# Optimization experiments

Hardware: AMD Instinct MI355X
Metric: run time of the kernel (lower is better)

The kernel has to match this reference:

```python
import jax, jax.numpy as jnp
import numpy as np

B, N, C, H = 8, 1024, 768, 12
D = C // H
SCALE = D ** -0.5


def setup_inputs() -> dict:
    key = jax.random.key(0)
    ks = jax.random.split(key, 6)
    std = 0.02
    return {
        "x": jax.random.normal(ks[0], (B, N, C), dtype=jnp.float32),
        "w_qkv": jax.random.normal(ks[1], (3 * C, C), dtype=jnp.float32) * std,
        "w_proj": jax.random.normal(ks[2], (C, C), dtype=jnp.float32) * std,
        "b_proj": jnp.zeros((C,), dtype=jnp.float32),
        "conv_l_w": jax.random.normal(ks[3], (H, H), dtype=jnp.float32) * std,
        "conv_w_w": jax.random.normal(ks[4], (H, H), dtype=jnp.float32) * std,
    }


def reference(x, w_qkv, w_proj, b_proj, conv_l_w, conv_w_w):
    Bx, Nx, Cx = x.shape
    # qkv projection: torch Linear uses x @ W^T
    qkv = (x @ w_qkv.T).reshape(Bx, Nx, 3, H, D)
    qkv = jnp.transpose(qkv, (2, 0, 3, 1, 4))  # [3, B, H, N, D]
    q, k, v = qkv[0], qkv[1], qkv[2]
    q = q * SCALE
    attn = jnp.einsum("bhnd,bhmd->bhnm", q, k)  # [B,H,N,N]
    # 1x1 conv across heads (conv_l)
    attn = jnp.einsum("oh,bhnm->bonm", conv_l_w, attn)
    attn = jax.nn.softmax(attn, axis=-1)
    # 1x1 conv across heads (conv_w)
    attn = jnp.einsum("oh,bhnm->bonm", conv_w_w, attn)
    out = jnp.einsum("bhnm,bhmd->bhnd", attn, v)
    out = jnp.transpose(out, (0, 2, 1, 3)).reshape(Bx, Nx, Cx)
    return out @ w_proj.T + b_proj
```

## Files before the change

kernel.cpp:

```cpp
#include <hip/hip_runtime.h>
#include <hip/hip_bf16.h>

typedef __attribute__((ext_vector_type(8))) short short8;
typedef __attribute__((ext_vector_type(4))) short short4v;
typedef __attribute__((ext_vector_type(4))) float float4v;

#define NB 8
#define NH 12
#define NN 1024
#define ND 64
#define NC 768

__device__ __forceinline__ short f2bf(float f) {
  __hip_bfloat16 h = __float2bfloat16(f);
  union { __hip_bfloat16 h; short s; } u; u.h = h; return u.s;
}
__device__ __forceinline__ unsigned pk2(float a, float b) {
  unsigned ua = (unsigned short)f2bf(a);
  unsigned ub = (unsigned short)f2bf(b);
  return ua | (ub << 16);
}

template<int MODE>
__global__ __launch_bounds__(256, 2)
void gemm_kernel(const void* __restrict__ Ap, const float* __restrict__ Bw,
                 const float* __restrict__ bias,
                 __hip_bfloat16* __restrict__ Qo, __hip_bfloat16* __restrict__ Ko,
                 __hip_bfloat16* __restrict__ VTo, float* __restrict__ Out)
{
  __shared__ short As[128 * 40];
  __shared__ short Bs[128 * 40];
  const int tid = threadIdx.x;
  const int w = tid >> 6, lane = tid & 63, lr = lane & 15, lg = lane >> 4;
  const int wr = w >> 1, wc = w & 1;
  const int n0 = blockIdx.x * 128, m0 = blockIdx.y * 128;

  float4v acc[4][4];
  #pragma unroll
  for (int i = 0; i < 4; i++)
    #pragma unroll
    for (int j = 0; j < 4; j++)
      acc[i][j] = (float4v){0.f, 0.f, 0.f, 0.f};

  for (int kt = 0; kt < 768; kt += 32) {
    if (MODE == 0) {
      const float* A = (const float*)Ap;
      #pragma unroll
      for (int i2 = 0; i2 < 4; i2++) {
        int c = tid + 256 * i2;
        int row = c >> 3, c4 = c & 7;
        float4v v = *(const float4v*)(A + (size_t)(m0 + row) * 768 + kt + c4 * 4);
        short4v s = { f2bf(v[0]), f2bf(v[1]), f2bf(v[2]), f2bf(v[3]) };
        *(short4v*)(&As[row * 40 + c4 * 4]) = s;
      }
    } else {
      const __hip_bfloat16* A = (const __hip_bfloat16*)Ap;
      #pragma unroll
      for (int i2 = 0; i2 < 2; i2++) {
        int c = tid + 256 * i2;
        int row = c >> 2, c8 = c & 3;
        *(short8*)(&As[row * 40 + c8 * 8]) =
            *(const short8*)(A + (size_t)(m0 + row) * 768 + kt + c8 * 8);
      }
    }
    #pragma unroll
    for (int i2 = 0; i2 < 4; i2++) {
      int c = tid + 256 * i2;
      int row = c >> 3, c4 = c & 7;
      float4v v = *(const float4v*)(Bw + (size_t)(n0 + row) * 768 + kt + c4 * 4);
      short4v s = { f2bf(v[0]), f2bf(v[1]), f2bf(v[2]), f2bf(v[3]) };
      *(short4v*)(&Bs[row * 40 + c4 * 4]) = s;
    }
    __syncthreads();

    short8 af[4], bfr[4];
    #pragma unroll
    for (int i = 0; i < 4; i++)
      af[i] = *(const short8*)(&As[(wr * 64 + i * 16 + lr) * 40 + lg * 8]);
    #pragma unroll
    for (int j = 0; j < 4; j++)
      bfr[j] = *(const short8*)(&Bs[(wc * 64 + j * 16 + lr) * 40 + lg * 8]);
    #pragma unroll
    for (int i = 0; i < 4; i++)
      #pragma unroll
      for (int j = 0; j < 4; j++)
        acc[i][j] = __builtin_amdgcn_mfma_f32_16x16x32_bf16(af[i], bfr[j], acc[i][j], 0, 0, 0);
    __syncthreads();
  }

  #pragma unroll
  for (int i = 0; i < 4; i++) {
    #pragma unroll
    for (int j = 0; j < 4; j++) {
      #pragma unroll
      for (int r = 0; r < 4; r++) {
        float val = acc[i][j][r];
        int mg_ = m0 + wr * 64 + i * 16 + lg * 4 + r;
        int ng_ = n0 + wc * 64 + j * 16 + lr;
        if (MODE == 0) {
          int s = ng_ / 768;
          int rem = ng_ - s * 768;
          int h = rem >> 6, d = rem & 63;
          int b = mg_ >> 10, n = mg_ & 1023;
          if (s == 0)
            Qo[(((size_t)b * NH + h) * NN + n) * ND + d] = __float2bfloat16(val * 0.125f);
          else if (s == 1)
            Ko[(((size_t)b * NH + h) * NN + n) * ND + d] = __float2bfloat16(val);
          else
            VTo[(((size_t)b * NH + h) * ND + d) * NN + n] = __float2bfloat16(val);
        } else {
          Out[(size_t)mg_ * NC + ng_] = val + bias[ng_];
        }
      }
    }
  }
}

__global__ __launch_bounds__(256, 2)
void attn_kernel(const __hip_bfloat16* __restrict__ Qg, const __hip_bfloat16* __restrict__ Kg,
                 const __hip_bfloat16* __restrict__ VTg,
                 const float* __restrict__ convl, const float* __restrict__ convw,
                 __hip_bfloat16* __restrict__ AOut)
{
  __shared__ short Sb[32 * 576];
  __shared__ short pm[16 * 648];
  __shared__ short lwA[512];
  __shared__ short wwT[512];

  const int tid = threadIdx.x;
  const int w = tid >> 6, lane = tid & 63, lr = lane & 15, lg = lane >> 4;
  const int b = blockIdx.x & 7;
  const int n0 = (blockIdx.x >> 3) * 16;
  const float4v zf = (float4v){0.f, 0.f, 0.f, 0.f};

  for (int i = tid; i < 512; i += 256) {
    int r = i >> 5, k = i & 31;
    bool v = (r < 12) && (k < 12);
    lwA[i] = v ? f2bf(convl[r * 12 + k]) : (short)0;
    wwT[i] = v ? f2bf(convw[r * 12 + k]) : (short)0;
  }
  for (int i = tid; i < 512; i += 256) {
    short* p = &Sb[i * 36 + 12];
    #pragma unroll
    for (int j = 0; j < 24; j++) p[j] = 0;
  }

  short8 qf[3][2];
  #pragma unroll
  for (int hh = 0; hh < 3; hh++)
    #pragma unroll
    for (int ks = 0; ks < 2; ks++)
      qf[hh][ks] = *(const short8*)(Qg +
          (((size_t)b * NH + w * 3 + hh) * NN + n0 + lr) * ND + ks * 32 + lg * 8);

  short8 kreg[3][2][2];
  auto loadK = [&](int t) {
    const int m0t = t * 32;
    #pragma unroll
    for (int hh = 0; hh < 3; hh++) {
      const size_t kbase = (((size_t)b * NH + w * 3 + hh) * NN + m0t) * ND;
      #pragma unroll
      for (int j = 0; j < 2; j++)
        #pragma unroll
        for (int ks = 0; ks < 2; ks++)
          kreg[hh][j][ks] = *(const short8*)(Kg + kbase +
              (size_t)(j * 16 + lr) * ND + ks * 32 + lg * 8);
    }
  };
  loadK(0);
  __syncthreads();
  const short8 lwf = *(const short8*)(&lwA[lr * 32 + lg * 8]);
  const short8 wwf = *(const short8*)(&wwT[lr * 32 + lg * 8]);

  float Lacc[4][4];
  #pragma unroll
  for (int r = 0; r < 4; r++)
    #pragma unroll
    for (int nn = 0; nn < 4; nn++) Lacc[r][nn] = 0.f;

  for (int t = 0; t < 32; t++) {
    #pragma unroll
    for (int hh = 0; hh < 3; hh++) {
      const int h = w * 3 + hh;
      #pragma unroll
      for (int j = 0; j < 2; j++) {
        float4v a = zf;
        #pragma unroll
        for (int ks = 0; ks < 2; ks++)
          a = __builtin_amdgcn_mfma_f32_16x16x32_bf16(qf[hh][ks], kreg[hh][j][ks], a, 0, 0, 0);
        #pragma unroll
        for (int r = 0; r < 4; r++)
          Sb[((lg * 4 + r) * 2 + j) * 576 + lr * 36 + h] = f2bf(a[r]);
      }
    }
    loadK(t < 31 ? t + 1 : 0);
    __syncthreads();
    #pragma unroll
    for (int cc = 0; cc < 8; cc++) {
      const int c = w * 8 + cc;
      short8 sb = *(const short8*)(&Sb[c * 576 + lr * 36 + lg * 8]);
      float4v d = __builtin_amdgcn_mfma_f32_16x16x32_bf16(lwf, sb, zf, 0, 0, 0);
      #pragma unroll
      for (int r = 0; r < 4; r++)
        Lacc[r][cc >> 1] += __expf(d[r]);
    }
    __syncthreads();
  }
  float logLreg[4][4];
  #pragma unroll
  for (int r = 0; r < 4; r++)
    #pragma unroll
    for (int nn = 0; nn < 4; nn++) {
      float v = Lacc[r][nn];
      v += __shfl_xor(v, 1);
      v += __shfl_xor(v, 2);
      v += __shfl_xor(v, 4);
      v += __shfl_xor(v, 8);
      logLreg[r][nn] = __logf(v);
    }

  float4v oacc[3][4];
  #pragma unroll
  for (int hh = 0; hh < 3; hh++)
    #pragma unroll
    for (int jd = 0; jd < 4; jd++) oacc[hh][jd] = zf;

  for (int t = 0; t <= 32; t++) {
    short8 vt0[3][2];
    if (t > 0) {
      const int m0v = (t - 1) * 32;
      #pragma unroll
      for (int hh = 0; hh < 3; hh++) {
        const size_t vbase = ((size_t)b * NH + w * 3 + hh) * ND * NN;
        #pragma unroll
        for (int jj = 0; jj < 2; jj++)
          vt0[hh][jj] = *(const short8*)(VTg + vbase +
              (size_t)(jj * 16 + lr) * NN + m0v + lg * 8);
      }
    }
    if (t < 32) {
      #pragma unroll
      for (int hh = 0; hh < 3; hh++) {
        const int h = w * 3 + hh;
        #pragma unroll
        for (int j = 0; j < 2; j++) {
          float4v a = zf;
          #pragma unroll
          for (int ks = 0; ks < 2; ks++)
            a = __builtin_amdgcn_mfma_f32_16x16x32_bf16(qf[hh][ks], kreg[hh][j][ks], a, 0, 0, 0);
          #pragma unroll
          for (int r = 0; r < 4; r++)
            Sb[((lg * 4 + r) * 2 + j) * 576 + lr * 36 + h] = f2bf(a[r]);
        }
      }
      if (t < 31) loadK(t + 1);
    }
    if (t > 0) {
      const int m0v = (t - 1) * 32;
      short8 pf[3];
      #pragma unroll
      for (int hh = 0; hh < 3; hh++)
        pf[hh] = *(const short8*)(&pm[(w * 3 + hh) * 648 + lr * 40 + lg * 8]);
      #pragma unroll
      for (int hh = 0; hh < 3; hh++)
        #pragma unroll
        for (int jj = 0; jj < 2; jj++)
          oacc[hh][jj] = __builtin_amdgcn_mfma_f32_16x16x32_bf16(vt0[hh][jj], pf[hh], oacc[hh][jj], 0, 0, 0);
      short8 vt1[3][2];
      #pragma unroll
      for (int hh = 0; hh < 3; hh++) {
        const size_t vbase = ((size_t)b * NH + w * 3 + hh) * ND * NN;
        #pragma unroll
        for (int jj = 0; jj < 2; jj++)
          vt1[hh][jj] = *(const short8*)(VTg + vbase +
              (size_t)((2 + jj) * 16 + lr) * NN + m0v + lg * 8);
      }
      #pragma unroll
      for (int hh = 0; hh < 3; hh++)
        #pragma unroll
        for (int jj = 0; jj < 2; jj++)
          oacc[hh][2 + jj] = __builtin_amdgcn_mfma_f32_16x16x32_bf16(vt1[hh][jj], pf[hh], oacc[hh][2 + jj], 0, 0, 0);
    }
    __syncthreads();
    if (t < 32) {
      #pragma unroll
      for (int cc = 0; cc < 8; cc++) {
        const int c = w * 8 + cc;
        short8 sb = *(const short8*)(&Sb[c * 576 + lr * 36 + lg * 8]);
        float4v d = __builtin_amdgcn_mfma_f32_16x16x32_bf16(lwf, sb, zf, 0, 0, 0);
        float p0 = __expf(d[0] - logLreg[0][cc >> 1]);
        float p1 = __expf(d[1] - logLreg[1][cc >> 1]);
        float p2 = __expf(d[2] - logLreg[2][cc >> 1]);
        float p3 = __expf(d[3] - logLreg[3][cc >> 1]);
        unsigned* dst = (unsigned*)(&Sb[c * 576 + lr * 36 + lg * 4]);
        dst[0] = pk2(p0, p1);
        dst[1] = pk2(p2, p3);
      }
      asm volatile("s_waitcnt lgkmcnt(0)" ::: "memory");
      __builtin_amdgcn_sched_barrier(0);
      #pragma unroll
      for (int cc = 0; cc < 8; cc++) {
        const int c = w * 8 + cc;
        short8 pb = *(const short8*)(&Sb[c * 576 + lr * 36 + lg * 8]);
        float4v d = __builtin_amdgcn_mfma_f32_16x16x32_bf16(pb, wwf, zf, 0, 0, 0);
        unsigned* dst = (unsigned*)(&pm[lr * 648 + (c >> 1) * 40 + (c & 1) * 16 + lg * 4]);
        dst[0] = pk2(d[0], d[1]);
        dst[1] = pk2(d[2], d[3]);
      }
    }
    __syncthreads();
  }

  #pragma unroll
  for (int hh = 0; hh < 3; hh++) {
    const int o2 = w * 3 + hh;
    #pragma unroll
    for (int jd = 0; jd < 4; jd++) {
      size_t base = ((size_t)b * NN + n0 + lr) * NC + o2 * 64 + jd * 16 + lg * 4;
      unsigned* dst = (unsigned*)(&AOut[base]);
      dst[0] = pk2(oacc[hh][jd][0], oacc[hh][jd][1]);
      dst[1] = pk2(oacc[hh][jd][2], oacc[hh][jd][3]);
    }
  }
}

extern "C" void kernel_launch(void* const* d_in, const int* in_sizes, int n_in,
                              void* d_out, int out_size, void* d_ws, size_t ws_size,
                              hipStream_t stream) {
  const float* x      = (const float*)d_in[0];
  const float* w_qkv  = (const float*)d_in[1];
  const float* w_proj = (const float*)d_in[2];
  const float* b_proj = (const float*)d_in[3];
  const float* conv_l = (const float*)d_in[4];
  const float* conv_w = (const float*)d_in[5];
  float* out = (float*)d_out;

  const size_t NE = (size_t)NB * NH * NN * ND;
  __hip_bfloat16* Qb = (__hip_bfloat16*)d_ws;
  __hip_bfloat16* Kb = Qb + NE;
  __hip_bfloat16* VT = Kb + NE;
  __hip_bfloat16* AO = VT + NE;

  gemm_kernel<0><<<dim3(18, 64), 256, 0, stream>>>(x, w_qkv, nullptr, Qb, Kb, VT, nullptr);
  attn_kernel<<<dim3(512), 256, 0, stream>>>(Qb, Kb, VT, conv_l, conv_w, AO);
  gemm_kernel<1><<<dim3(6, 64), 256, 0, stream>>>(AO, w_proj, b_proj, nullptr, nullptr, nullptr, out);
}
```

Before: 392.0 us.

## Prefetch V tiles one iteration ahead, use raw barriers and MFMA priority hints

Issues the V-transpose global loads for the next PV step during the softmax/conv phase, so they overlap with LDS and exp work instead of stalling right before the MFMAs. Replaces __syncthreads with an explicit lgkmcnt wait plus s_barrier that does not wait on outstanding global loads. Also raises wave priority around the MFMA sections. This raises register pressure by holding 12 short8 V fragments across the loop. The hand-written barrier also depends on vmcnt not being needed at those points.

```diff
diff --git a/kernel.cpp b/kernel.cpp
--- a/kernel.cpp
+++ b/kernel.cpp
@@ -10,6 +10,11 @@
 #define NN 1024
 #define ND 64
 #define NC 768
+
+#define RAWBAR() do { \
+  asm volatile("s_waitcnt lgkmcnt(0)" ::: "memory"); \
+  __builtin_amdgcn_s_barrier(); \
+} while (0)
 
 __device__ __forceinline__ short f2bf(float f) {
   __hip_bfloat16 h = __float2bfloat16(f);
@@ -167,8 +172,21 @@
               (size_t)(j * 16 + lr) * ND + ks * 32 + lg * 8);
     }
   };
+  short8 vt[3][4];
+  auto loadVT = [&](int t) {
+    const int m0v = t * 32;
+    #pragma unroll
+    for (int hh = 0; hh < 3; hh++) {
+      const size_t vbase = ((size_t)b * NH + w * 3 + hh) * ND * NN;
+      #pragma unroll
+      for (int jd = 0; jd < 4; jd++)
+        vt[hh][jd] = *(const short8*)(VTg + vbase +
+            (size_t)(jd * 16 + lr) * NN + m0v + lg * 8);
+    }
+  };
+
   loadK(0);
-  __syncthreads();
+  RAWBAR();
   const short8 lwf = *(const short8*)(&lwA[lr * 32 + lg * 8]);
   const short8 wwf = *(const short8*)(&wwT[lr * 32 + lg * 8]);
 
@@ -179,6 +197,7 @@
     for (int nn = 0; nn < 4; nn++) Lacc[r][nn] = 0.f;
 
   for (int t = 0; t < 32; t++) {
+    __builtin_amdgcn_s_setprio(1);
     #pragma unroll
     for (int hh = 0; hh < 3; hh++) {
       const int h = w * 3 + hh;
@@ -193,8 +212,9 @@
           Sb[((lg * 4 + r) * 2 + j) * 576 + lr * 36 + h] = f2bf(a[r]);
       }
     }
+    __builtin_amdgcn_s_setprio(0);
     loadK(t < 31 ? t + 1 : 0);
-    __syncthreads();
+    RAWBAR();
     #pragma unroll
     for (int cc = 0; cc < 8; cc++) {
       const int c = w * 8 + cc;
@@ -204,7 +224,7 @@
       for (int r = 0; r < 4; r++)
         Lacc[r][cc >> 1] += __expf(d[r]);
     }
-    __syncthreads();
+    RAWBAR();
   }
   float logLreg[4][4];
   #pragma unroll
@@ -226,18 +246,13 @@
     for (int jd = 0; jd < 4; jd++) oacc[hh][jd] = zf;
 
   for (int t = 0; t <= 32; t++) {
-    short8 vt0[3][2];
+    short8 pf[3];
     if (t > 0) {
-      const int m0v = (t - 1) * 32;
-      #pragma unroll
-      for (int hh = 0; hh < 3; hh++) {
-        const size_t vbase = ((size_t)b * NH + w * 3 + hh) * ND * NN;
-        #pragma unroll
-        for (int jj = 0; jj < 2; jj++)
-          vt0[hh][jj] = *(const short8*)(VTg + vbase +
-              (size_t)(jj * 16 + lr) * NN + m0v + lg * 8);
-      }
-    }
+      #pragma unroll
+      for (int hh = 0; hh < 3; hh++)
+        pf[hh] = *(const short8*)(&pm[(w * 3 + hh) * 648 + lr * 40 + lg * 8]);
+    }
+    __builtin_amdgcn_s_setprio(1);
     if (t < 32) {
       #pragma unroll
       for (int hh = 0; hh < 3; hh++) {
@@ -256,33 +271,16 @@
       if (t < 31) loadK(t + 1);
     }
     if (t > 0) {
-      const int m0v = (t - 1) * 32;
-      short8 pf[3];
       #pragma unroll
       for (int hh = 0; hh < 3; hh++)
-        pf[hh] = *(const short8*)(&pm[(w * 3 + hh) * 648 + lr * 40 + lg * 8]);
-      #pragma unroll
-      for (int hh = 0; hh < 3; hh++)
-        #pragma unroll
-        for (int jj = 0; jj < 2; jj++)
-          oacc[hh][jj] = __builtin_amdgcn_mfma_f32_16x16x32_bf16(vt0[hh][jj], pf[hh], oacc[hh][jj], 0, 0, 0);
-      short8 vt1[3][2];
-      #pragma unroll
-      for (int hh = 0; hh < 3; hh++) {
-        const size_t vbase = ((size_t)b * NH + w * 3 + hh) * ND * NN;
-        #pragma unroll
-        for (int jj = 0; jj < 2; jj++)
-          vt1[hh][jj] = *(const short8*)(VTg + vbase +
-              (size_t)((2 + jj) * 16 + lr) * NN + m0v + lg * 8);
-      }
-      #pragma unroll
-      for (int hh = 0; hh < 3; hh++)
-        #pragma unroll
-        for (int jj = 0; jj < 2; jj++)
-          oacc[hh][2 + jj] = __builtin_amdgcn_mfma_f32_16x16x32_bf16(vt1[hh][jj], pf[hh], oacc[hh][2 + jj], 0, 0, 0);
-    }
-    __syncthreads();
+        #pragma unroll
+        for (int jd = 0; jd < 4; jd++)
+          oacc[hh][jd] = __builtin_amdgcn_mfma_f32_16x16x32_bf16(vt[hh][jd], pf[hh], oacc[hh][jd], 0, 0, 0);
+    }
+    __builtin_amdgcn_s_setprio(0);
+    RAWBAR();
     if (t < 32) {
+      loadVT(t);
       #pragma unroll
       for (int cc = 0; cc < 8; cc++) {
         const int c = w * 8 + cc;
@@ -308,7 +306,7 @@
         dst[1] = pk2(d[2], d[3]);
       }
     }
-    __syncthreads();
+    RAWBAR();
   }
 
   #pragma unroll
```

After: 375.5 us. 1.04x faster.
